# Performance work log

Hardware: AMD Instinct MI355X
Metric: run time of the kernel (lower is better)

The kernel has to match this reference:

```python
import jax, jax.numpy as jnp
import numpy as np

HIDDEN = 1024
HEADS = 16
HEAD_DIM = HIDDEN // HEADS

def setup_inputs() -> dict:
    key = jax.random.key(0)
    ks = jax.random.split(key, 11)
    B, T, D = 2, 2048, HIDDEN
    s = 1.0 / np.sqrt(D)
    return {
        "query": jax.random.normal(ks[0], (B, T, D), jnp.float32),
        "key": jax.random.normal(ks[1], (B, T, D), jnp.float32),
        "value": jax.random.normal(ks[2], (B, T, D), jnp.float32),
        "Wq": jax.random.normal(ks[3], (D, D), jnp.float32) * s,
        "bq": jnp.zeros((D,), jnp.float32),
        "Wk": jax.random.normal(ks[4], (D, D), jnp.float32) * s,
        "bk": jnp.zeros((D,), jnp.float32),
        "Wv": jax.random.normal(ks[5], (D, D), jnp.float32) * s,
        "bv": jnp.zeros((D,), jnp.float32),
        "Wo": jax.random.normal(ks[6], (D, D), jnp.float32) * s,
        "bo": jnp.zeros((D,), jnp.float32),
    }

def reference(query, key, value, Wq, bq, Wk, bk, Wv, bv, Wo, bo):
    B, Tq, D = query.shape
    Tk = key.shape[1]
    H, Hd = HEADS, HEAD_DIM
    # projections -> [B, H, T, Hd]
    Q = (query @ Wq + bq).reshape(B, Tq, H, Hd).transpose(0, 2, 1, 3)
    K = (key @ Wk + bk).reshape(B, Tk, H, Hd).transpose(0, 2, 1, 3)
    V = (value @ Wv + bv).reshape(B, Tk, H, Hd).transpose(0, 2, 1, 3)
    scale = jnp.sqrt(jnp.asarray(Hd, Q.dtype))
    scores = jnp.einsum('bhqd,bhkd->bhqk', Q, K) / scale  # [B,H,Tq,Tk]
    causal = jnp.triu(jnp.ones((Tq, Tk), bool), k=1)
    scores = jnp.where(causal[None, None], jnp.asarray(-jnp.inf, scores.dtype), scores)
    attn = jax.nn.softmax(scores, axis=-1)
    out = jnp.einsum('bhqk,bhkd->bhqd', attn, V)  # [B,H,Tq,Hd]
    out = out.transpose(0, 2, 1, 3).reshape(B, Tq, D)
    return out @ Wo + bo
```

## Files before the change

kernel.cpp:

```cpp
#include <hip/hip_runtime.h>
#include <hip/hip_bf16.h>


typedef __bf16 bf16_t;
typedef __bf16 bf16x8 __attribute__((ext_vector_type(8)));
typedef float f32x4 __attribute__((ext_vector_type(4)));
typedef unsigned int u32;

#define D_MODEL 1024
#define SEQ_T   2048
#define NHEAD   16
#define HDIM    64
#define M_ROWS  4096
#define MEGA    (1024 * 1024)

__device__ __forceinline__ void gl2lds16(const void* g, void* l) {
    __builtin_amdgcn_global_load_lds((const __attribute__((address_space(1))) u32*)g,
                                     (__attribute__((address_space(3))) u32*)l, 16, 0, 0);
}

__global__ __launch_bounds__(256) void prep(
    const float* __restrict__ Wq, const float* __restrict__ Wk,
    const float* __restrict__ Wv, const float* __restrict__ Wo,
    const float* __restrict__ Xq, const float* __restrict__ Xk, const float* __restrict__ Xv,
    bf16_t* __restrict__ Wqt, bf16_t* __restrict__ Wkt,
    bf16_t* __restrict__ Wvt, bf16_t* __restrict__ Wot,
    bf16_t* __restrict__ Xb)
{
    int blk = blockIdx.x, tid = threadIdx.x;
    if (blk < 4096) {
        int wi = blk >> 10, t = blk & 1023;
        int n0 = (t & 31) * 32, k0 = (t >> 5) * 32;
        const float* W = wi == 0 ? Wq : (wi == 1 ? Wk : (wi == 2 ? Wv : Wo));
        bf16_t* Wt = wi == 0 ? Wqt : (wi == 1 ? Wkt : (wi == 2 ? Wvt : Wot));
        __shared__ float tile[32][33];
        int tx = tid & 31, ty = tid >> 5;
#pragma unroll
        for (int i = 0; i < 32; i += 8)
            tile[ty + i][tx] = W[(k0 + ty + i) * D_MODEL + n0 + tx];
        __syncthreads();
#pragma unroll
        for (int i = 0; i < 32; i += 8)
            Wt[(size_t)(n0 + ty + i) * D_MODEL + k0 + tx] = (bf16_t)tile[tx][ty + i];
    } else {
        int b2 = blk - 4096;
        int xi = b2 >> 10;
        const float* X = xi == 0 ? Xq : (xi == 1 ? Xk : Xv);
        bf16_t* XB = Xb + (size_t)xi * M_ROWS * D_MODEL;
        size_t base = (size_t)(b2 & 1023) * 4096 + tid * 16;
        const float4* xp = (const float4*)(X + base);
        float4 a0 = xp[0], a1 = xp[1], a2 = xp[2], a3 = xp[3];
        bf16x8 o0, o1;
        o0[0] = (bf16_t)a0.x; o0[1] = (bf16_t)a0.y; o0[2] = (bf16_t)a0.z; o0[3] = (bf16_t)a0.w;
        o0[4] = (bf16_t)a1.x; o0[5] = (bf16_t)a1.y; o0[6] = (bf16_t)a1.z; o0[7] = (bf16_t)a1.w;
        o1[0] = (bf16_t)a2.x; o1[1] = (bf16_t)a2.y; o1[2] = (bf16_t)a2.z; o1[3] = (bf16_t)a2.w;
        o1[4] = (bf16_t)a3.x; o1[5] = (bf16_t)a3.y; o1[6] = (bf16_t)a3.z; o1[7] = (bf16_t)a3.w;
        *(bf16x8*)(XB + base) = o0;
        *(bf16x8*)(XB + base + 8) = o1;
    }
}

template <bool PRECAST>
__global__ __launch_bounds__(256) void proj_fused(
    const float* __restrict__ Xq, const float* __restrict__ Xk, const float* __restrict__ Xv,
    const bf16_t* __restrict__ Xb,
    const bf16_t* __restrict__ Wqt, const bf16_t* __restrict__ Wkt, const bf16_t* __restrict__ Wvt,
    const float* __restrict__ bq, const float* __restrict__ bk, const float* __restrict__ bv,
    bf16_t* __restrict__ Qh, bf16_t* __restrict__ Kh, bf16_t* __restrict__ Vt)
{
    __shared__ bf16_t Ab[128 * 32];
    __shared__ bf16_t Bb[128 * 32];
    int tid = threadIdx.x;
    int w = tid >> 6, lane = tid & 63, lo16 = lane & 15, quad = lane >> 4;
    int m0 = blockIdx.x * 128;
    int proj = blockIdx.y >> 3;
    int n0 = (blockIdx.y & 7) * 128;
    const float*  X    = proj == 0 ? Xq  : (proj == 1 ? Xk  : Xv);
    const bf16_t* XB   = Xb + (size_t)proj * M_ROWS * D_MODEL;
    const bf16_t* Wt   = proj == 0 ? Wqt : (proj == 1 ? Wkt : Wvt);
    const float*  bias = proj == 0 ? bq  : (proj == 1 ? bk  : bv);
    int wm = (w >> 1) * 64, wn = (w & 1) * 64;

    f32x4 acc[4][4];
#pragma unroll
    for (int i = 0; i < 4; i++)
#pragma unroll
        for (int j = 0; j < 4; j++) acc[i][j] = (f32x4){0.f, 0.f, 0.f, 0.f};

    for (int k0 = 0; k0 < D_MODEL; k0 += 32) {
        __syncthreads();
#pragma unroll
        for (int p = 0; p < 2; p++) {
            int idx = p * 256 + tid;
            int row = idx >> 2, ch = (idx & 3) * 8;
            if (PRECAST) {
                gl2lds16(XB + (size_t)(m0 + row) * D_MODEL + k0 + ch, Ab + idx * 8);
            } else {
                const float* as = X + (size_t)(m0 + row) * D_MODEL + k0 + ch;
                float4 a0 = *(const float4*)as, a1 = *(const float4*)(as + 4);
                bf16x8 av;
                av[0] = (bf16_t)a0.x; av[1] = (bf16_t)a0.y; av[2] = (bf16_t)a0.z; av[3] = (bf16_t)a0.w;
                av[4] = (bf16_t)a1.x; av[5] = (bf16_t)a1.y; av[6] = (bf16_t)a1.z; av[7] = (bf16_t)a1.w;
                *(bf16x8*)(Ab + idx * 8) = av;
            }
            gl2lds16(Wt + (size_t)(n0 + row) * D_MODEL + k0 + ch, Bb + idx * 8);
        }
        __syncthreads();
        bf16x8 af[4], bfr[4];
#pragma unroll
        for (int i = 0; i < 4; i++)
            af[i] = *(bf16x8*)(Ab + (wm + i * 16 + lo16) * 32 + quad * 8);
#pragma unroll
        for (int j = 0; j < 4; j++)
            bfr[j] = *(bf16x8*)(Bb + (wn + j * 16 + lo16) * 32 + quad * 8);
#pragma unroll
        for (int i = 0; i < 4; i++)
#pragma unroll
            for (int j = 0; j < 4; j++)
                acc[i][j] = __builtin_amdgcn_mfma_f32_16x16x32_bf16(af[i], bfr[j], acc[i][j], 0, 0, 0);
    }

    float qscale = proj == 0 ? 0.1803368801111244f : 1.0f;
#pragma unroll
    for (int j = 0; j < 4; j++) {
        int col = n0 + wn + j * 16 + lo16;
        float bv2 = bias[col];
        int h = col >> 6, hd = col & 63;
#pragma unroll
        for (int i = 0; i < 4; i++) {
#pragma unroll
            for (int r = 0; r < 4; r++) {
                int m = m0 + wm + i * 16 + quad * 4 + r;
                int b = m >> 11, t = m & 2047;
                bf16_t val = (bf16_t)((acc[i][j][r] + bv2) * qscale);
                if (proj == 2)
                    Vt[(((size_t)(b * NHEAD + h) * HDIM + hd) * SEQ_T) + t] = val;
                else if (proj == 1)
                    Kh[(((size_t)(b * NHEAD + h) * SEQ_T + t) * HDIM) + hd] = val;
                else
                    Qh[(((size_t)(b * NHEAD + h) * SEQ_T + t) * HDIM) + hd] = val;
            }
        }
    }
}

__global__ __launch_bounds__(256, 2) void flash_attn(const bf16_t* __restrict__ Qh,
                                                     const bf16_t* __restrict__ Kh,
                                                     const bf16_t* __restrict__ Vt,
                                                     bf16_t* __restrict__ Ob) {
    int bh = blockIdx.x & 31;
    int qt = 15 - (int)(blockIdx.x >> 5);
    int tid = threadIdx.x;
    int w = tid >> 6, lane = tid & 63, lo16 = lane & 15, quad = lane >> 4;
    int qbase = qt * 128 + w * 32;

    __shared__ bf16_t KL[2][64 * 64];
    __shared__ bf16_t VL[2][64 * 64];
    __shared__ bf16_t PL[4][32 * 64];
    bf16_t* myP = PL[w];

    const bf16_t* Qp = Qh + (size_t)bh * SEQ_T * HDIM;
    const bf16_t* Kp = Kh + (size_t)bh * SEQ_T * HDIM;
    const bf16_t* Vp = Vt + (size_t)bh * HDIM * SEQ_T;

    bf16x8 qf[2][2];
#pragma unroll
    for (int m = 0; m < 2; m++) {
        const bf16_t* qr = Qp + (size_t)(qbase + m * 16 + lo16) * HDIM;
        qf[m][0] = *(const bf16x8*)(qr + quad * 8);
        qf[m][1] = *(const bf16x8*)(qr + 32 + quad * 8);
    }

    bf16x8 ones;
#pragma unroll
    for (int i = 0; i < 8; i++) ones[i] = (bf16_t)1.0f;

    f32x4 oacc[2][4], lacc[2];
#pragma unroll
    for (int m = 0; m < 2; m++) {
        lacc[m] = (f32x4){0.f, 0.f, 0.f, 0.f};
#pragma unroll
        for (int s = 0; s < 4; s++) oacc[m][s] = (f32x4){0.f, 0.f, 0.f, 0.f};
    }

    int nkt = 2 * (qt + 1);
    int myNkt = 2 * qt + 1 + (w >> 1);

#pragma unroll
    for (int p = 0; p < 2; p++) {
        int idx = p * 256 + tid;
        int row = idx >> 3, cp = idx & 7, cl = (cp - row) & 7;
        gl2lds16(Kp + (size_t)row * HDIM + cl * 8, KL[0] + idx * 8);
        gl2lds16(Vp + (size_t)row * SEQ_T + cl * 8, VL[0] + idx * 8);
    }

    for (int kt = 0; kt < nkt; kt++) {
        int cur = kt & 1;
        __syncthreads();

        if (kt + 1 < nkt) {
#pragma unroll
            for (int p = 0; p < 2; p++) {
                int idx = p * 256 + tid;
                int row = idx >> 3, cp = idx & 7, cl = (cp - row) & 7;
                gl2lds16(Kp + (size_t)((kt + 1) * 64 + row) * HDIM + cl * 8, KL[cur ^ 1] + idx * 8);
                gl2lds16(Vp + (size_t)row * SEQ_T + (kt + 1) * 64 + cl * 8, VL[cur ^ 1] + idx * 8);
            }
        }

        if (kt >= myNkt) continue;
        const bf16_t* KLc = KL[cur];
        const bf16_t* VLc = VL[cur];

        f32x4 sacc[2][4];
#pragma unroll
        for (int m = 0; m < 2; m++)
#pragma unroll
            for (int s = 0; s < 4; s++) sacc[m][s] = (f32x4){0.f, 0.f, 0.f, 0.f};
#pragma unroll
        for (int s = 0; s < 4; s++) {
            int keyl = s * 16 + lo16;
            bf16x8 kf0 = *(const bf16x8*)(KLc + keyl * 64 + ((quad + keyl) & 7) * 8);
            bf16x8 kf1 = *(const bf16x8*)(KLc + keyl * 64 + ((quad + 4 + keyl) & 7) * 8);
#pragma unroll
            for (int m = 0; m < 2; m++) {
                sacc[m][s] = __builtin_amdgcn_mfma_f32_16x16x32_bf16(qf[m][0], kf0, sacc[m][s], 0, 0, 0);
                sacc[m][s] = __builtin_amdgcn_mfma_f32_16x16x32_bf16(qf[m][1], kf1, sacc[m][s], 0, 0, 0);
            }
        }

        bool diag = (kt == myNkt - 1);
        bf16x8 pf[2][2];
#pragma unroll
        for (int m = 0; m < 2; m++) {
#pragma unroll
            for (int s = 0; s < 4; s++) {
                int col = s * 16 + lo16;
#pragma unroll
                for (int r = 0; r < 4; r++) {
                    int rowl = m * 16 + quad * 4 + r;
                    float p = exp2f(sacc[m][s][r]);
                    if (diag) {
                        int key = kt * 64 + col, qq = qbase + rowl;
                        p = (key <= qq) ? p : 0.f;
                    }
                    int phys = ((col >> 3) + rowl + (rowl >> 3)) & 7;
                    myP[rowl * 64 + phys * 8 + (col & 7)] = (bf16_t)p;
                }
            }
            int rowA = m * 16 + lo16;
            int Rr = (rowA + (rowA >> 3)) & 7;
            pf[m][0] = *(bf16x8*)(myP + rowA * 64 + ((quad + Rr) & 7) * 8);
            pf[m][1] = *(bf16x8*)(myP + rowA * 64 + ((quad + 4 + Rr) & 7) * 8);
            lacc[m] = __builtin_amdgcn_mfma_f32_16x16x32_bf16(pf[m][0], ones, lacc[m], 0, 0, 0);
            lacc[m] = __builtin_amdgcn_mfma_f32_16x16x32_bf16(pf[m][1], ones, lacc[m], 0, 0, 0);
        }

#pragma unroll
        for (int s = 0; s < 4; s++) {
            int dl = s * 16 + lo16;
            bf16x8 vf0 = *(const bf16x8*)(VLc + dl * 64 + ((quad + dl) & 7) * 8);
            bf16x8 vf1 = *(const bf16x8*)(VLc + dl * 64 + ((quad + 4 + dl) & 7) * 8);
#pragma unroll
            for (int m = 0; m < 2; m++) {
                oacc[m][s] = __builtin_amdgcn_mfma_f32_16x16x32_bf16(pf[m][0], vf0, oacc[m][s], 0, 0, 0);
                oacc[m][s] = __builtin_amdgcn_mfma_f32_16x16x32_bf16(pf[m][1], vf1, oacc[m][s], 0, 0, 0);
            }
        }
    }

    int b = bh >> 4, h = bh & 15;
#pragma unroll
    for (int m = 0; m < 2; m++)
#pragma unroll
        for (int s = 0; s < 4; s++) {
            int d = s * 16 + lo16;
#pragma unroll
            for (int r = 0; r < 4; r++) {
                int q = qbase + m * 16 + quad * 4 + r;
                float o = oacc[m][s][r] / lacc[m][r];
                Ob[((size_t)b * SEQ_T + q) * D_MODEL + h * HDIM + d] = (bf16_t)o;
            }
        }
}

__global__ __launch_bounds__(256) void out_gemm(const bf16_t* __restrict__ A,
                                                const bf16_t* __restrict__ Wt,
                                                const float* __restrict__ bias,
                                                float* __restrict__ out) {
    __shared__ bf16_t Ab[128 * 32];
    __shared__ bf16_t Bb[128 * 32];
    int tid = threadIdx.x;
    int w = tid >> 6, lane = tid & 63, lo16 = lane & 15, quad = lane >> 4;
    int m0 = blockIdx.x * 128;
    int n0 = blockIdx.y * 128;
    int wm = (w >> 1) * 64, wn = (w & 1) * 64;

    f32x4 acc[4][4];
#pragma unroll
    for (int i = 0; i < 4; i++)
#pragma unroll
        for (int j = 0; j < 4; j++) acc[i][j] = (f32x4){0.f, 0.f, 0.f, 0.f};

    for (int k0 = 0; k0 < D_MODEL; k0 += 32) {
        __syncthreads();
#pragma unroll
        for (int p = 0; p < 2; p++) {
            int idx = p * 256 + tid;
            int row = idx >> 2, ch = (idx & 3) * 8;
            gl2lds16(A  + (size_t)(m0 + row) * D_MODEL + k0 + ch, Ab + idx * 8);
            gl2lds16(Wt + (size_t)(n0 + row) * D_MODEL + k0 + ch, Bb + idx * 8);
        }
        __syncthreads();
        bf16x8 af[4], bfr[4];
#pragma unroll
        for (int i = 0; i < 4; i++)
            af[i] = *(bf16x8*)(Ab + (wm + i * 16 + lo16) * 32 + quad * 8);
#pragma unroll
        for (int j = 0; j < 4; j++)
            bfr[j] = *(bf16x8*)(Bb + (wn + j * 16 + lo16) * 32 + quad * 8);
#pragma unroll
        for (int i = 0; i < 4; i++)
#pragma unroll
            for (int j = 0; j < 4; j++)
                acc[i][j] = __builtin_amdgcn_mfma_f32_16x16x32_bf16(af[i], bfr[j], acc[i][j], 0, 0, 0);
    }

#pragma unroll
    for (int j = 0; j < 4; j++) {
        int col = n0 + wn + j * 16 + lo16;
        float bv2 = bias[col];
#pragma unroll
        for (int i = 0; i < 4; i++)
#pragma unroll
            for (int r = 0; r < 4; r++) {
                int m = m0 + wm + i * 16 + quad * 4 + r;
                out[(size_t)m * D_MODEL + col] = acc[i][j][r] + bv2;
            }
    }
}

extern "C" void kernel_launch(void* const* d_in, const int* in_sizes, int n_in,
                              void* d_out, int out_size, void* d_ws, size_t ws_size,
                              hipStream_t stream) {
    const float* q  = (const float*)d_in[0];
    const float* k  = (const float*)d_in[1];
    const float* v  = (const float*)d_in[2];
    const float* Wq = (const float*)d_in[3];
    const float* bq = (const float*)d_in[4];
    const float* Wk = (const float*)d_in[5];
    const float* bk = (const float*)d_in[6];
    const float* Wv = (const float*)d_in[7];
    const float* bv = (const float*)d_in[8];
    const float* Wo = (const float*)d_in[9];
    const float* bo = (const float*)d_in[10];
    float* out = (float*)d_out;

    bf16_t* Wqt = (bf16_t*)d_ws;
    bf16_t* Wkt = Wqt + (size_t)MEGA;
    bf16_t* Wvt = Wkt + (size_t)MEGA;
    bf16_t* Wot = Wvt + (size_t)MEGA;
    bf16_t* Qh  = Wot + (size_t)MEGA;
    bf16_t* Kh  = Qh  + (size_t)M_ROWS * D_MODEL;
    bf16_t* Vt  = Kh  + (size_t)M_ROWS * D_MODEL;
    bf16_t* Xb  = Vt  + (size_t)M_ROWS * D_MODEL;
    bf16_t* Ob  = Xb;

    bool precast = ws_size >= (size_t)(4 * MEGA + 3 * M_ROWS * D_MODEL + 3 * M_ROWS * D_MODEL) * sizeof(bf16_t);

    int prep_blocks = precast ? 4096 + 3 * 1024 : 4096;
    prep<<<prep_blocks, 256, 0, stream>>>(Wq, Wk, Wv, Wo, q, k, v, Wqt, Wkt, Wvt, Wot, Xb);

    dim3 pg(M_ROWS / 128, 24);
    if (precast)
        proj_fused<true><<<pg, 256, 0, stream>>>(q, k, v, Xb, Wqt, Wkt, Wvt, bq, bk, bv, Qh, Kh, Vt);
    else
        proj_fused<false><<<pg, 256, 0, stream>>>(q, k, v, Xb, Wqt, Wkt, Wvt, bq, bk, bv, Qh, Kh, Vt);

    flash_attn<<<32 * 16, 256, 0, stream>>>(Qh, Kh, Vt, Ob);

    dim3 og(M_ROWS / 128, D_MODEL / 128);
    out_gemm<<<og, 256, 0, stream>>>(Ob, Wot, bo, out);
}
```

Measured before the change: 237.2 us.

## Use 32x32 MFMA with register P in attention, deepen GEMM K tiles with swizzle

The attention kernel moves to 32x32x16 MFMA with a transposed S=K·Q^T layout. The probability tile is now rebuilt in registers via permlane32_swap instead of a round trip through LDS, and the kernel launches 1024 blocks of 128 threads with an interleaved tile order for causal load balance. The projection and output GEMMs double the K step to 64 with an XOR-style swizzled LDS layout, halving the barriers per K. This raises register pressure and LDS per block and depends on the permlane32 builtin being available on this target.

```diff
diff --git a/kernel.cpp b/kernel.cpp
--- a/kernel.cpp
+++ b/kernel.cpp
@@ -5,7 +5,10 @@
 typedef __bf16 bf16_t;
 typedef __bf16 bf16x8 __attribute__((ext_vector_type(8)));
 typedef float f32x4 __attribute__((ext_vector_type(4)));
+typedef float f32x16 __attribute__((ext_vector_type(16)));
 typedef unsigned int u32;
+typedef unsigned int u32x2v __attribute__((ext_vector_type(2)));
+typedef unsigned int u32x4v __attribute__((ext_vector_type(4)));
 
 #define D_MODEL 1024
 #define SEQ_T   2048
@@ -17,6 +20,12 @@
 __device__ __forceinline__ void gl2lds16(const void* g, void* l) {
     __builtin_amdgcn_global_load_lds((const __attribute__((address_space(1))) u32*)g,
                                      (__attribute__((address_space(3))) u32*)l, 16, 0, 0);
+}
+
+__device__ __forceinline__ u32 pk2(float a, float b) {
+    unsigned short x = __builtin_bit_cast(unsigned short, (bf16_t)a);
+    unsigned short y = __builtin_bit_cast(unsigned short, (bf16_t)b);
+    return (u32)x | ((u32)y << 16);
 }
 
 __global__ __launch_bounds__(256) void prep(
@@ -68,8 +77,8 @@
     const float* __restrict__ bq, const float* __restrict__ bk, const float* __restrict__ bv,
     bf16_t* __restrict__ Qh, bf16_t* __restrict__ Kh, bf16_t* __restrict__ Vt)
 {
-    __shared__ bf16_t Ab[128 * 32];
-    __shared__ bf16_t Bb[128 * 32];
+    __shared__ bf16_t Ab[128 * 64];
+    __shared__ bf16_t Bb[128 * 64];
     int tid = threadIdx.x;
     int w = tid >> 6, lane = tid & 63, lo16 = lane & 15, quad = lane >> 4;
     int m0 = blockIdx.x * 128;
@@ -87,37 +96,44 @@
 #pragma unroll
         for (int j = 0; j < 4; j++) acc[i][j] = (f32x4){0.f, 0.f, 0.f, 0.f};
 
-    for (int k0 = 0; k0 < D_MODEL; k0 += 32) {
-        __syncthreads();
-#pragma unroll
-        for (int p = 0; p < 2; p++) {
+    for (int k0 = 0; k0 < D_MODEL; k0 += 64) {
+        __syncthreads();
+#pragma unroll
+        for (int p = 0; p < 4; p++) {
             int idx = p * 256 + tid;
-            int row = idx >> 2, ch = (idx & 3) * 8;
+            int row = idx >> 3, cp = idx & 7, cl = (cp - row) & 7;
             if (PRECAST) {
-                gl2lds16(XB + (size_t)(m0 + row) * D_MODEL + k0 + ch, Ab + idx * 8);
+                gl2lds16(XB + (size_t)(m0 + row) * D_MODEL + k0 + cl * 8, Ab + idx * 8);
             } else {
-                const float* as = X + (size_t)(m0 + row) * D_MODEL + k0 + ch;
+                const float* as = X + (size_t)(m0 + row) * D_MODEL + k0 + cl * 8;
                 float4 a0 = *(const float4*)as, a1 = *(const float4*)(as + 4);
                 bf16x8 av;
                 av[0] = (bf16_t)a0.x; av[1] = (bf16_t)a0.y; av[2] = (bf16_t)a0.z; av[3] = (bf16_t)a0.w;
                 av[4] = (bf16_t)a1.x; av[5] = (bf16_t)a1.y; av[6] = (bf16_t)a1.z; av[7] = (bf16_t)a1.w;
                 *(bf16x8*)(Ab + idx * 8) = av;
             }
-            gl2lds16(Wt + (size_t)(n0 + row) * D_MODEL + k0 + ch, Bb + idx * 8);
-        }
-        __syncthreads();
-        bf16x8 af[4], bfr[4];
-#pragma unroll
-        for (int i = 0; i < 4; i++)
-            af[i] = *(bf16x8*)(Ab + (wm + i * 16 + lo16) * 32 + quad * 8);
-#pragma unroll
-        for (int j = 0; j < 4; j++)
-            bfr[j] = *(bf16x8*)(Bb + (wn + j * 16 + lo16) * 32 + quad * 8);
-#pragma unroll
-        for (int i = 0; i < 4; i++)
-#pragma unroll
-            for (int j = 0; j < 4; j++)
-                acc[i][j] = __builtin_amdgcn_mfma_f32_16x16x32_bf16(af[i], bfr[j], acc[i][j], 0, 0, 0);
+            gl2lds16(Wt + (size_t)(n0 + row) * D_MODEL + k0 + cl * 8, Bb + idx * 8);
+        }
+        __syncthreads();
+#pragma unroll
+        for (int kk = 0; kk < 2; kk++) {
+            bf16x8 af[4], bfr[4];
+#pragma unroll
+            for (int i = 0; i < 4; i++) {
+                int row = wm + i * 16 + lo16;
+                af[i] = *(bf16x8*)(Ab + row * 64 + ((4 * kk + quad + row) & 7) * 8);
+            }
+#pragma unroll
+            for (int j = 0; j < 4; j++) {
+                int row = wn + j * 16 + lo16;
+                bfr[j] = *(bf16x8*)(Bb + row * 64 + ((4 * kk + quad + row) & 7) * 8);
+            }
+#pragma unroll
+            for (int i = 0; i < 4; i++)
+#pragma unroll
+                for (int j = 0; j < 4; j++)
+                    acc[i][j] = __builtin_amdgcn_mfma_f32_16x16x32_bf16(af[i], bfr[j], acc[i][j], 0, 0, 0);
+        }
     }
 
     float qscale = proj == 0 ? 0.1803368801111244f : 1.0f;
@@ -144,51 +160,48 @@
     }
 }
 
-__global__ __launch_bounds__(256, 2) void flash_attn(const bf16_t* __restrict__ Qh,
+__global__ __launch_bounds__(128, 2) void flash_attn(const bf16_t* __restrict__ Qh,
                                                      const bf16_t* __restrict__ Kh,
                                                      const bf16_t* __restrict__ Vt,
                                                      bf16_t* __restrict__ Ob) {
-    int bh = blockIdx.x & 31;
-    int qt = 15 - (int)(blockIdx.x >> 5);
+    int blk = blockIdx.x;
+    int bh = blk & 31;
+    int s5 = blk >> 5;
+    int seg = s5 >> 3, o = s5 & 7;
+    int j = seg == 0 ? 31 - o : (seg == 1 ? 16 + o : (seg == 2 ? 15 - o : o));
     int tid = threadIdx.x;
-    int w = tid >> 6, lane = tid & 63, lo16 = lane & 15, quad = lane >> 4;
-    int qbase = qt * 128 + w * 32;
+    int w = tid >> 6, lane = tid & 63;
+    int l32 = lane & 31, hi = lane >> 5;
+    int qbase = j * 64 + w * 32;
 
     __shared__ bf16_t KL[2][64 * 64];
     __shared__ bf16_t VL[2][64 * 64];
-    __shared__ bf16_t PL[4][32 * 64];
-    bf16_t* myP = PL[w];
 
     const bf16_t* Qp = Qh + (size_t)bh * SEQ_T * HDIM;
     const bf16_t* Kp = Kh + (size_t)bh * SEQ_T * HDIM;
     const bf16_t* Vp = Vt + (size_t)bh * HDIM * SEQ_T;
 
-    bf16x8 qf[2][2];
-#pragma unroll
-    for (int m = 0; m < 2; m++) {
-        const bf16_t* qr = Qp + (size_t)(qbase + m * 16 + lo16) * HDIM;
-        qf[m][0] = *(const bf16x8*)(qr + quad * 8);
-        qf[m][1] = *(const bf16x8*)(qr + 32 + quad * 8);
+    bf16x8 qf[4];
+    {
+        const bf16_t* qr = Qp + (size_t)(qbase + l32) * HDIM;
+#pragma unroll
+        for (int kd = 0; kd < 4; kd++)
+            qf[kd] = *(const bf16x8*)(qr + kd * 16 + hi * 8);
     }
 
     bf16x8 ones;
 #pragma unroll
     for (int i = 0; i < 8; i++) ones[i] = (bf16_t)1.0f;
 
-    f32x4 oacc[2][4], lacc[2];
-#pragma unroll
-    for (int m = 0; m < 2; m++) {
-        lacc[m] = (f32x4){0.f, 0.f, 0.f, 0.f};
-#pragma unroll
-        for (int s = 0; s < 4; s++) oacc[m][s] = (f32x4){0.f, 0.f, 0.f, 0.f};
-    }
-
-    int nkt = 2 * (qt + 1);
-    int myNkt = 2 * qt + 1 + (w >> 1);
-
-#pragma unroll
-    for (int p = 0; p < 2; p++) {
-        int idx = p * 256 + tid;
+    f32x16 oacc[2], lacc;
+#pragma unroll
+    for (int r = 0; r < 16; r++) { oacc[0][r] = 0.f; oacc[1][r] = 0.f; lacc[r] = 0.f; }
+
+    int nkt = j + 1;
+
+#pragma unroll
+    for (int p = 0; p < 4; p++) {
+        int idx = p * 128 + tid;
         int row = idx >> 3, cp = idx & 7, cl = (cp - row) & 7;
         gl2lds16(Kp + (size_t)row * HDIM + cl * 8, KL[0] + idx * 8);
         gl2lds16(Vp + (size_t)row * SEQ_T + cl * 8, VL[0] + idx * 8);
@@ -200,87 +213,80 @@
 
         if (kt + 1 < nkt) {
 #pragma unroll
-            for (int p = 0; p < 2; p++) {
-                int idx = p * 256 + tid;
+            for (int p = 0; p < 4; p++) {
+                int idx = p * 128 + tid;
                 int row = idx >> 3, cp = idx & 7, cl = (cp - row) & 7;
                 gl2lds16(Kp + (size_t)((kt + 1) * 64 + row) * HDIM + cl * 8, KL[cur ^ 1] + idx * 8);
                 gl2lds16(Vp + (size_t)row * SEQ_T + (kt + 1) * 64 + cl * 8, VL[cur ^ 1] + idx * 8);
             }
         }
-
-        if (kt >= myNkt) continue;
         const bf16_t* KLc = KL[cur];
         const bf16_t* VLc = VL[cur];
 
-        f32x4 sacc[2][4];
-#pragma unroll
-        for (int m = 0; m < 2; m++)
-#pragma unroll
-            for (int s = 0; s < 4; s++) sacc[m][s] = (f32x4){0.f, 0.f, 0.f, 0.f};
-#pragma unroll
-        for (int s = 0; s < 4; s++) {
-            int keyl = s * 16 + lo16;
-            bf16x8 kf0 = *(const bf16x8*)(KLc + keyl * 64 + ((quad + keyl) & 7) * 8);
-            bf16x8 kf1 = *(const bf16x8*)(KLc + keyl * 64 + ((quad + 4 + keyl) & 7) * 8);
-#pragma unroll
-            for (int m = 0; m < 2; m++) {
-                sacc[m][s] = __builtin_amdgcn_mfma_f32_16x16x32_bf16(qf[m][0], kf0, sacc[m][s], 0, 0, 0);
-                sacc[m][s] = __builtin_amdgcn_mfma_f32_16x16x32_bf16(qf[m][1], kf1, sacc[m][s], 0, 0, 0);
-            }
-        }
-
-        bool diag = (kt == myNkt - 1);
-        bf16x8 pf[2][2];
-#pragma unroll
-        for (int m = 0; m < 2; m++) {
-#pragma unroll
-            for (int s = 0; s < 4; s++) {
-                int col = s * 16 + lo16;
-#pragma unroll
-                for (int r = 0; r < 4; r++) {
-                    int rowl = m * 16 + quad * 4 + r;
-                    float p = exp2f(sacc[m][s][r]);
-                    if (diag) {
-                        int key = kt * 64 + col, qq = qbase + rowl;
-                        p = (key <= qq) ? p : 0.f;
-                    }
-                    int phys = ((col >> 3) + rowl + (rowl >> 3)) & 7;
-                    myP[rowl * 64 + phys * 8 + (col & 7)] = (bf16_t)p;
+        f32x16 sacc[2];
+#pragma unroll
+        for (int r = 0; r < 16; r++) { sacc[0][r] = 0.f; sacc[1][r] = 0.f; }
+#pragma unroll
+        for (int ks = 0; ks < 2; ks++) {
+            int key = l32 + 32 * ks;
+#pragma unroll
+            for (int kd = 0; kd < 4; kd++) {
+                bf16x8 kf = *(const bf16x8*)(KLc + key * 64 + ((2 * kd + hi + key) & 7) * 8);
+                sacc[ks] = __builtin_amdgcn_mfma_f32_32x32x16_bf16(kf, qf[kd], sacc[ks], 0, 0, 0);
+            }
+        }
+
+        bool diag = (kt == nkt - 1);
+        int qg = qbase + l32;
+#pragma unroll
+        for (int ks = 0; ks < 2; ks++)
+#pragma unroll
+            for (int r = 0; r < 16; r++) {
+                float e = exp2f(sacc[ks][r]);
+                if (diag) {
+                    int key = kt * 64 + ks * 32 + (r & 3) + 8 * (r >> 2) + 4 * hi;
+                    e = (key <= qg) ? e : 0.f;
                 }
-            }
-            int rowA = m * 16 + lo16;
-            int Rr = (rowA + (rowA >> 3)) & 7;
-            pf[m][0] = *(bf16x8*)(myP + rowA * 64 + ((quad + Rr) & 7) * 8);
-            pf[m][1] = *(bf16x8*)(myP + rowA * 64 + ((quad + 4 + Rr) & 7) * 8);
-            lacc[m] = __builtin_amdgcn_mfma_f32_16x16x32_bf16(pf[m][0], ones, lacc[m], 0, 0, 0);
-            lacc[m] = __builtin_amdgcn_mfma_f32_16x16x32_bf16(pf[m][1], ones, lacc[m], 0, 0, 0);
-        }
-
-#pragma unroll
-        for (int s = 0; s < 4; s++) {
-            int dl = s * 16 + lo16;
-            bf16x8 vf0 = *(const bf16x8*)(VLc + dl * 64 + ((quad + dl) & 7) * 8);
-            bf16x8 vf1 = *(const bf16x8*)(VLc + dl * 64 + ((quad + 4 + dl) & 7) * 8);
-#pragma unroll
-            for (int m = 0; m < 2; m++) {
-                oacc[m][s] = __builtin_amdgcn_mfma_f32_16x16x32_bf16(pf[m][0], vf0, oacc[m][s], 0, 0, 0);
-                oacc[m][s] = __builtin_amdgcn_mfma_f32_16x16x32_bf16(pf[m][1], vf1, oacc[m][s], 0, 0, 0);
+                sacc[ks][r] = e;
+            }
+
+        bf16x8 pf[4];
+#pragma unroll
+        for (int t = 0; t < 4; t++) {
+            const int ks = t >> 1, bb = (t & 1) * 8;
+            u32 A1 = pk2(sacc[ks][bb + 0], sacc[ks][bb + 1]);
+            u32 A2 = pk2(sacc[ks][bb + 2], sacc[ks][bb + 3]);
+            u32 C1 = pk2(sacc[ks][bb + 4], sacc[ks][bb + 5]);
+            u32 C2 = pk2(sacc[ks][bb + 6], sacc[ks][bb + 7]);
+            u32x2v s1 = __builtin_amdgcn_permlane32_swap(A1, C1, false, false);
+            u32x2v s2 = __builtin_amdgcn_permlane32_swap(A2, C2, false, false);
+            u32x4v wv; wv[0] = s1[0]; wv[1] = s2[0]; wv[2] = s1[1]; wv[3] = s2[1];
+            pf[t] = __builtin_bit_cast(bf16x8, wv);
+            lacc = __builtin_amdgcn_mfma_f32_32x32x16_bf16(pf[t], ones, lacc, 0, 0, 0);
+        }
+
+#pragma unroll
+        for (int dt = 0; dt < 2; dt++) {
+            int d = l32 + 32 * dt;
+#pragma unroll
+            for (int t = 0; t < 4; t++) {
+                bf16x8 vf = *(const bf16x8*)(VLc + d * 64 + ((2 * t + hi + d) & 7) * 8);
+                oacc[dt] = __builtin_amdgcn_mfma_f32_32x32x16_bf16(pf[t], vf, oacc[dt], 0, 0, 0);
             }
         }
     }
 
     int b = bh >> 4, h = bh & 15;
-#pragma unroll
-    for (int m = 0; m < 2; m++)
-#pragma unroll
-        for (int s = 0; s < 4; s++) {
-            int d = s * 16 + lo16;
-#pragma unroll
-            for (int r = 0; r < 4; r++) {
-                int q = qbase + m * 16 + quad * 4 + r;
-                float o = oacc[m][s][r] / lacc[m][r];
-                Ob[((size_t)b * SEQ_T + q) * D_MODEL + h * HDIM + d] = (bf16_t)o;
-            }
+    float inv[16];
+#pragma unroll
+    for (int r = 0; r < 16; r++) inv[r] = 1.0f / lacc[r];
+#pragma unroll
+    for (int dt = 0; dt < 2; dt++)
+#pragma unroll
+        for (int r = 0; r < 16; r++) {
+            int q = qbase + (r & 3) + 8 * (r >> 2) + 4 * hi;
+            int d = l32 + 32 * dt;
+            Ob[((size_t)b * SEQ_T + q) * D_MODEL + h * HDIM + d] = (bf16_t)(oacc[dt][r] * inv[r]);
         }
 }
 
@@ -288,8 +294,8 @@
                                                 const bf16_t* __restrict__ Wt,
                                                 const float* __restrict__ bias,
                                                 float* __restrict__ out) {
-    __shared__ bf16_t Ab[128 * 32];
-    __shared__ bf16_t Bb[128 * 32];
+    __shared__ bf16_t Ab[128 * 64];
+    __shared__ bf16_t Bb[128 * 64];
     int tid = threadIdx.x;
     int w = tid >> 6, lane = tid & 63, lo16 = lane & 15, quad = lane >> 4;
     int m0 = blockIdx.x * 128;
@@ -302,28 +308,35 @@
 #pragma unroll
         for (int j = 0; j < 4; j++) acc[i][j] = (f32x4){0.f, 0.f, 0.f, 0.f};
 
-    for (int k0 = 0; k0 < D_MODEL; k0 += 32) {
-        __syncthreads();
-#pragma unroll
-        for (int p = 0; p < 2; p++) {
+    for (int k0 = 0; k0 < D_MODEL; k0 += 64) {
+        __syncthreads();
+#pragma unroll
+        for (int p = 0; p < 4; p++) {
             int idx = p * 256 + tid;
-            int row = idx >> 2, ch = (idx & 3) * 8;
-            gl2lds16(A  + (size_t)(m0 + row) * D_MODEL + k0 + ch, Ab + idx * 8);
-            gl2lds16(Wt + (size_t)(n0 + row) * D_MODEL + k0 + ch, Bb + idx * 8);
-        }
-        __syncthreads();
-        bf16x8 af[4], bfr[4];
-#pragma unroll
-        for (int i = 0; i < 4; i++)
-            af[i] = *(bf16x8*)(Ab + (wm + i * 16 + lo16) * 32 + quad * 8);
-#pragma unroll
-        for (int j = 0; j < 4; j++)
-            bfr[j] = *(bf16x8*)(Bb + (wn + j * 16 + lo16) * 32 + quad * 8);
-#pragma unroll
-        for (int i = 0; i < 4; i++)
-#pragma unroll
-            for (int j = 0; j < 4; j++)
-                acc[i][j] = __builtin_amdgcn_mfma_f32_16x16x32_bf16(af[i], bfr[j], acc[i][j], 0, 0, 0);
+            int row = idx >> 3, cp = idx & 7, cl = (cp - row) & 7;
+            gl2lds16(A  + (size_t)(m0 + row) * D_MODEL + k0 + cl * 8, Ab + idx * 8);
+            gl2lds16(Wt + (size_t)(n0 + row) * D_MODEL + k0 + cl * 8, Bb + idx * 8);
+        }
+        __syncthreads();
+#pragma unroll
+        for (int kk = 0; kk < 2; kk++) {
+            bf16x8 af[4], bfr[4];
+#pragma unroll
+            for (int i = 0; i < 4; i++) {
+                int row = wm + i * 16 + lo16;
+                af[i] = *(bf16x8*)(Ab + row * 64 + ((4 * kk + quad + row) & 7) * 8);
+            }
+#pragma unroll
+            for (int j = 0; j < 4; j++) {
+                int row = wn + j * 16 + lo16;
+                bfr[j] = *(bf16x8*)(Bb + row * 64 + ((4 * kk + quad + row) & 7) * 8);
+            }
+#pragma unroll
+            for (int i = 0; i < 4; i++)
+#pragma unroll
+                for (int j = 0; j < 4; j++)
+                    acc[i][j] = __builtin_amdgcn_mfma_f32_16x16x32_bf16(af[i], bfr[j], acc[i][j], 0, 0, 0);
+        }
     }
 
 #pragma unroll
@@ -377,7 +390,7 @@
     else
         proj_fused<false><<<pg, 256, 0, stream>>>(q, k, v, Xb, Wqt, Wkt, Wvt, bq, bk, bv, Qh, Kh, Vt);
 
-    flash_attn<<<32 * 16, 256, 0, stream>>>(Qh, Kh, Vt, Ob);
+    flash_attn<<<32 * 32, 128, 0, stream>>>(Qh, Kh, Vt, Ob);
 
     dim3 og(M_ROWS / 128, D_MODEL / 128);
     out_gemm<<<og, 256, 0, stream>>>(Ob, Wot, bo, out);
```

Result: slower. 245.2 us (+3.4%).
